# Optimization experiments

Hardware: AMD Instinct MI355X
Metric: run time of the kernel (lower is better)

The kernel has to match this reference:

```python
import jax, jax.numpy as jnp
import numpy as np

N = 4096          # n_assets
D_MODEL = 512
DK = 128
EMB_DIM = 32
QC = 4.0          # quantization_coeff
NUM_EMB = int(np.floor((N - 1) / QC)) + 1  # 1024


def setup_inputs() -> dict:
    key = jax.random.key(0)
    ks = jax.random.split(key, 9)

    def lin_w(k, out_d, in_d):
        # torch nn.Linear default init ~ U(-1/sqrt(in_d), 1/sqrt(in_d))
        b = 1.0 / np.sqrt(in_d)
        return jax.random.uniform(k, (out_d, in_d), jnp.float32, -b, b)

    return {
        "stock_reprs": jax.random.normal(ks[0], (N, D_MODEL), jnp.float32),
        "price_rising_ranks": jax.random.uniform(ks[1], (N,), jnp.float32, 0.0, float(N)),
        "Wq_w": lin_w(ks[2], DK, D_MODEL), "Wq_b": jnp.zeros((DK,), jnp.float32),
        "Wk_w": lin_w(ks[3], DK, D_MODEL), "Wk_b": jnp.zeros((DK,), jnp.float32),
        "Wv_w": lin_w(ks[4], D_MODEL, D_MODEL), "Wv_b": jnp.zeros((D_MODEL,), jnp.float32),
        "rank_emb": jax.random.normal(ks[5], (NUM_EMB, EMB_DIM), jnp.float32),
        "wL_w": lin_w(ks[6], 1, EMB_DIM), "wL_b": jnp.zeros((1,), jnp.float32),
        "wf_w": lin_w(ks[7], 1, D_MODEL), "wf_b": jnp.zeros((1,), jnp.float32),
    }


def reference(stock_reprs, price_rising_ranks, Wq_w, Wq_b, Wk_w, Wk_b,
              Wv_w, Wv_b, rank_emb, wL_w, wL_b, wf_w, wf_b):
    # QKV projections: [N, dk], [N, dk], [N, d_model]
    q = stock_reprs @ Wq_w.T + Wq_b
    k = stock_reprs @ Wk_w.T + Wk_b
    v = stock_reprs @ Wv_w.T + Wv_b

    # Quantized pairwise rank-distance indices [N, N]
    diff = jnp.abs(price_rising_ranks[:, None] - price_rising_ranks[None, :])
    d_ij = jnp.clip(jnp.floor(diff / QC).astype(jnp.int32), 0, NUM_EMB - 1)

    # Gate per quantized distance: sigmoid(w_L(Emb[d])). Precompute the
    # [NUM_EMB] table instead of materializing the [N, N, EMB_DIM] gather
    # (same math: the lookup-then-linear commutes with the gather).
    gate_table = jax.nn.sigmoid(rank_emb @ wL_w[0] + wL_b[0])  # [NUM_EMB]
    psi = gate_table[d_ij]                                     # [N, N]

    score = (q @ k.T) / np.sqrt(float(DK))                     # [N, N]
    att = jax.nn.softmax(psi * score, axis=-1)                 # [N, N]
    a = att @ v                                                # [N, d_model]
    return jax.nn.sigmoid(a @ wf_w[0] + wf_b[0])               # [N]
```

## Files before the change

### kernel.cpp

```cpp
#include <hip/hip_runtime.h>
#include <hip/hip_bf16.h>

#define N_ASSETS 4096
#define DMODEL 512
#define DKQ 128
#define NUM_EMB 1024

#define SCLQ 0.12752789f

typedef float f32x4 __attribute__((ext_vector_type(4)));
typedef short s16x8 __attribute__((ext_vector_type(8)));

__device__ __forceinline__ unsigned short f2bf(float x) {
    unsigned u = __float_as_uint(x);
    u += 0x7FFF + ((u >> 16) & 1);
    return (unsigned short)(u >> 16);
}

__device__ __forceinline__ unsigned pk2(float lo, float hi) {
    __hip_bfloat162 h = __float22bfloat162_rn(make_float2(lo, hi));
    return *(unsigned*)&h;
}

__device__ __forceinline__ s16x8 ld8(const unsigned short* p) {
    return *(const s16x8*)p;
}

__global__ __launch_bounds__(256) void k_prep(const float* __restrict__ remb,
                                              const float* __restrict__ wLw,
                                              const float* __restrict__ wLb,
                                              const float* __restrict__ Wq,
                                              const float* __restrict__ Wk,
                                              const float* __restrict__ bq,
                                              const float* __restrict__ bk,
                                              const float* __restrict__ Wv,
                                              const float* __restrict__ bv,
                                              const float* __restrict__ wfw,
                                              float* __restrict__ gate,
                                              unsigned short* __restrict__ Wb,
                                              float* __restrict__ bias,
                                              float* __restrict__ weff4) {
    int bid = blockIdx.x;
    int tid = threadIdx.x;
    if (bid < 4) {
        int e = bid * 256 + tid;
        float s = wLb[0];
#pragma unroll
        for (int j = 0; j < 32; ++j) s += remb[e * 32 + j] * wLw[j];
        gate[e] = 1.f / (1.f + __expf(-s));
    } else if (bid < 132) {
        int gid = (bid - 4) * 256 + tid;
        int i4 = gid * 4;
        int row = i4 >> 9;
        int col = i4 & 511;
        const float* src; int r;
        if (row < 128) { src = Wq; r = row; } else { src = Wk; r = row - 128; }
        float4 v = *(const float4*)(src + r * 512 + col);
        ushort4 o;
        o.x = f2bf(v.x); o.y = f2bf(v.y); o.z = f2bf(v.z); o.w = f2bf(v.w);
        *(ushort4*)(Wb + i4) = o;
        if (gid < 256) bias[gid] = (gid < 128) ? bq[gid] : bk[gid - 128];
    } else if (bid < 136) {
        int dbase = (bid - 132) * 128;
        float a0 = 0.f, a1 = 0.f;
        const float* wp = Wv + (size_t)dbase * 512 + tid * 2;
#pragma unroll 8
        for (int j = 0; j < 128; ++j) {
            float wfv = wfw[dbase + j];
            float2 v = *(const float2*)(wp + (size_t)j * 512);
            a0 += v.x * wfv;
            a1 += v.y * wfv;
        }
        weff4[(bid - 132) * 512 + tid * 2] = a0;
        weff4[(bid - 132) * 512 + tid * 2 + 1] = a1;
    } else {
        if (tid < 64) {
            float s = 0.f;
#pragma unroll
            for (int j = 0; j < 8; ++j) s += bv[tid * 8 + j] * wfw[tid * 8 + j];
#pragma unroll
            for (int m = 1; m < 64; m <<= 1) s += __shfl_xor(s, m);
            if (tid == 0) weff4[2048] = s;
        }
    }
}

__global__ __launch_bounds__(256) void k_proj(const float* __restrict__ X,
                                              const float* __restrict__ weff4,
                                              const unsigned short* __restrict__ Wb,
                                              const float* __restrict__ bias,
                                              unsigned short* __restrict__ qb,
                                              unsigned short* __restrict__ kb,
                                              float* __restrict__ u) {
    int tid = threadIdx.x;
    int lane = tid & 63, w = tid >> 6;
    int l15 = lane & 15, lhi = lane >> 4;
    int m0 = blockIdx.x * 16;
    int n0w = blockIdx.y * 128 + w * 32;

    const float* xrow = X + (size_t)(m0 + l15) * DMODEL + lhi * 8;

    s16x8 af[16];
    float us = 0.f;
    bool dou = (w == 0) && (blockIdx.y == 0);
#pragma unroll
    for (int kc = 0; kc < 16; ++kc) {
        float4 a = *(const float4*)(xrow + kc * 32);
        float4 b = *(const float4*)(xrow + kc * 32 + 4);
        if (dou) {
            int off = kc * 32 + lhi * 8;
            float4 p0 = *(const float4*)(weff4 + off);
            float4 p1 = *(const float4*)(weff4 + 512 + off);
            float4 p2 = *(const float4*)(weff4 + 1024 + off);
            float4 p3 = *(const float4*)(weff4 + 1536 + off);
            float4 q0 = *(const float4*)(weff4 + off + 4);
            float4 q1 = *(const float4*)(weff4 + 512 + off + 4);
            float4 q2 = *(const float4*)(weff4 + 1024 + off + 4);
            float4 q3 = *(const float4*)(weff4 + 1536 + off + 4);
            float wax = p0.x + p1.x + p2.x + p3.x;
            float way = p0.y + p1.y + p2.y + p3.y;
            float waz = p0.z + p1.z + p2.z + p3.z;
            float waw = p0.w + p1.w + p2.w + p3.w;
            float wbx = q0.x + q1.x + q2.x + q3.x;
            float wby = q0.y + q1.y + q2.y + q3.y;
            float wbz = q0.z + q1.z + q2.z + q3.z;
            float wbw = q0.w + q1.w + q2.w + q3.w;
            us += a.x * wax + a.y * way + a.z * waz + a.w * waw
                + b.x * wbx + b.y * wby + b.z * wbz + b.w * wbw;
        }
        union { s16x8 v; unsigned q[4]; } fr;
        fr.q[0] = pk2(a.x, a.y);
        fr.q[1] = pk2(a.z, a.w);
        fr.q[2] = pk2(b.x, b.y);
        fr.q[3] = pk2(b.z, b.w);
        af[kc] = fr.v;
    }
    if (dou) {
        us += __shfl_xor(us, 16);
        us += __shfl_xor(us, 32);
        if (lane < 16) u[m0 + lane] = us + weff4[2048];
    }

    f32x4 zero4 = {0.f, 0.f, 0.f, 0.f};
    f32x4 acc[2];
#pragma unroll
    for (int ni = 0; ni < 2; ++ni) acc[ni] = zero4;

#pragma unroll
    for (int k0 = 0; k0 < 16; ++k0) {
#pragma unroll
        for (int ni = 0; ni < 2; ++ni) {
            s16x8 bf = ld8(Wb + (size_t)(n0w + ni * 16 + l15) * 512 + k0 * 32 + lhi * 8);
            acc[ni] = __builtin_amdgcn_mfma_f32_16x16x32_bf16(af[k0], bf, acc[ni], 0, 0, 0);
        }
    }

#pragma unroll
    for (int ni = 0; ni < 2; ++ni) {
        int n = n0w + ni * 16 + l15;
        float bv_ = bias[n];
#pragma unroll
        for (int r = 0; r < 4; ++r) {
            int m = m0 + lhi * 4 + r;
            float v = acc[ni][r] + bv_;
            if (n < 128) qb[m * 128 + n] = f2bf(v * SCLQ);
            else         kb[m * 128 + (n - 128)] = f2bf(v);
        }
    }
}

__global__ __launch_bounds__(256) void k_score(const unsigned short* __restrict__ qb,
                                               const unsigned short* __restrict__ kb,
                                               const float* __restrict__ ranks,
                                               const float* __restrict__ gate,
                                               const float* __restrict__ u,
                                               float* __restrict__ num_part,
                                               float* __restrict__ den_part) {
    __shared__ float g_lds[NUM_EMB];
    __shared__ float rr[128], rc[128], uc[128];
    int tid = threadIdx.x;
    int lane = tid & 63, w = tid >> 6;
    int l15 = lane & 15, lhi = lane >> 4;
    int wm = w >> 1, wn = w & 1;
    int bm = blockIdx.x, bn = blockIdx.y;

    for (int i = tid; i < NUM_EMB; i += 256) g_lds[i] = gate[i];
    if (tid < 128) {
        rr[tid] = ranks[bm * 128 + tid];
        rc[tid] = ranks[bn * 128 + tid];
        uc[tid] = u[bn * 128 + tid];
    }
    __syncthreads();

    int row0 = wm * 64;
    int col0 = wn * 64;

    f32x4 zero4 = {0.f, 0.f, 0.f, 0.f};
    f32x4 acc[4][4];
#pragma unroll
    for (int mi = 0; mi < 4; ++mi)
#pragma unroll
        for (int ni = 0; ni < 4; ++ni) acc[mi][ni] = zero4;

#pragma unroll
    for (int k0 = 0; k0 < DKQ; k0 += 32) {
        s16x8 af[4], bf[4];
#pragma unroll
        for (int mi = 0; mi < 4; ++mi)
            af[mi] = ld8(qb + (bm * 128 + row0 + mi * 16 + l15) * DKQ + k0 + lhi * 8);
#pragma unroll
        for (int ni = 0; ni < 4; ++ni)
            bf[ni] = ld8(kb + (bn * 128 + col0 + ni * 16 + l15) * DKQ + k0 + lhi * 8);
#pragma unroll
        for (int mi = 0; mi < 4; ++mi)
#pragma unroll
            for (int ni = 0; ni < 4; ++ni)
                acc[mi][ni] = __builtin_amdgcn_mfma_f32_16x16x32_bf16(af[mi], bf[ni], acc[mi][ni], 0, 0, 0);
    }

    float rreg[4][4];
#pragma unroll
    for (int mi = 0; mi < 4; ++mi)
#pragma unroll
        for (int r = 0; r < 4; ++r) rreg[mi][r] = rr[row0 + mi * 16 + lhi * 4 + r];

    float num[4][4], den[4][4];
#pragma unroll
    for (int mi = 0; mi < 4; ++mi)
#pragma unroll
        for (int r = 0; r < 4; ++r) { num[mi][r] = 0.f; den[mi][r] = 0.f; }

#pragma unroll
    for (int mi = 0; mi < 4; ++mi) {
#pragma unroll
        for (int ni = 0; ni < 4; ++ni) {
            int coll = col0 + ni * 16 + l15;
            float rj = rc[coll];
            float uj = uc[coll];
#pragma unroll
            for (int r = 0; r < 4; ++r) {
                float diff = fabsf(rreg[mi][r] - rj);
                int d = min((int)(diff * 0.25f), NUM_EMB - 1);
                float p = exp2f(g_lds[d] * acc[mi][ni][r]);
                den[mi][r] += p;
                num[mi][r] += p * uj;
            }
        }
    }
    int slot = bn * 2 + wn;
#pragma unroll
    for (int mi = 0; mi < 4; ++mi) {
#pragma unroll
        for (int r = 0; r < 4; ++r) {
            float vn = num[mi][r], vd = den[mi][r];
            vn += __shfl_xor(vn, 1); vd += __shfl_xor(vd, 1);
            vn += __shfl_xor(vn, 2); vd += __shfl_xor(vd, 2);
            vn += __shfl_xor(vn, 4); vd += __shfl_xor(vd, 4);
            vn += __shfl_xor(vn, 8); vd += __shfl_xor(vd, 8);
            if (l15 == 0) {
                int row = bm * 128 + row0 + mi * 16 + lhi * 4 + r;
                num_part[row * 64 + slot] = vn;
                den_part[row * 64 + slot] = vd;
            }
        }
    }
}

__global__ __launch_bounds__(256) void k_out(const float* __restrict__ num_part,
                                             const float* __restrict__ den_part,
                                             const float* __restrict__ wfb,
                                             float* __restrict__ out) {
    int lane = threadIdx.x & 63, w = threadIdx.x >> 6;
    int row = blockIdx.x * 4 + w;
    float vn = num_part[row * 64 + lane];
    float vd = den_part[row * 64 + lane];
#pragma unroll
    for (int m = 1; m < 64; m <<= 1) {
        vn += __shfl_xor(vn, m);
        vd += __shfl_xor(vd, m);
    }
    if (lane == 0) out[row] = 1.f / (1.f + __expf(-(vn / vd + wfb[0])));
}

extern "C" void kernel_launch(void* const* d_in, const int* in_sizes, int n_in,
                              void* d_out, int out_size, void* d_ws, size_t ws_size,
                              hipStream_t stream) {
    const float* X    = (const float*)d_in[0];
    const float* rks  = (const float*)d_in[1];
    const float* Wq_w = (const float*)d_in[2];
    const float* Wq_b = (const float*)d_in[3];
    const float* Wk_w = (const float*)d_in[4];
    const float* Wk_b = (const float*)d_in[5];
    const float* Wv_w = (const float*)d_in[6];
    const float* Wv_b = (const float*)d_in[7];
    const float* remb = (const float*)d_in[8];
    const float* wL_w = (const float*)d_in[9];
    const float* wL_b = (const float*)d_in[10];
    const float* wf_w = (const float*)d_in[11];
    const float* wf_b = (const float*)d_in[12];
    float* out = (float*)d_out;
    char* ws = (char*)d_ws;

    const size_t OFF_GATE  = 0;
    const size_t OFF_BIAS  = 4096;
    const size_t OFF_WEFF4 = 8192;
    const size_t OFF_WB    = 20480;
    const size_t OFF_QB    = OFF_WB + 262144;
    const size_t OFF_KB    = OFF_QB + 1048576;
    const size_t OFF_U     = OFF_KB + 1048576;
    const size_t OFF_NUM   = OFF_U + 16384;
    const size_t OFF_DEN   = OFF_NUM + 1048576;

    float* gate = (float*)(ws + OFF_GATE);
    float* bias = (float*)(ws + OFF_BIAS);
    float* weff4 = (float*)(ws + OFF_WEFF4);
    unsigned short* Wb = (unsigned short*)(ws + OFF_WB);
    unsigned short* qb = (unsigned short*)(ws + OFF_QB);
    unsigned short* kb = (unsigned short*)(ws + OFF_KB);
    float* u = (float*)(ws + OFF_U);
    float* num_part = (float*)(ws + OFF_NUM);
    float* den_part = (float*)(ws + OFF_DEN);

    k_prep<<<137, 256, 0, stream>>>(remb, wL_w, wL_b, Wq_w, Wk_w, Wq_b, Wk_b,
                                    Wv_w, Wv_b, wf_w, gate, Wb, bias, weff4);
    k_proj<<<dim3(256, 2), 256, 0, stream>>>(X, weff4, Wb, bias, qb, kb, u);
    k_score<<<dim3(32, 32), 256, 0, stream>>>(qb, kb, rks, gate, u, num_part, den_part);
    k_out<<<1024, 256, 0, stream>>>(num_part, den_part, wf_b, out);
}
```

Before: 60.18 us.

## Fuse final row reduction into score kernel via last-block atomic counter

Removes the separate k_out launch. Each score block bumps a per-row-block atomic counter, and the last of the 32 column blocks reduces the partial num/den sums and writes the sigmoid output, which needs a memset of the counters first. Also pre-scales the ranks by 0.25 so the quantised index is just the truncated absolute difference, dropping the min clamp, and splits the Wv·wf prep across more blocks so it runs in more parallel.

```diff
diff --git a/kernel.cpp b/kernel.cpp
--- a/kernel.cpp
+++ b/kernel.cpp
@@ -60,19 +60,20 @@
         o.x = f2bf(v.x); o.y = f2bf(v.y); o.z = f2bf(v.z); o.w = f2bf(v.w);
         *(ushort4*)(Wb + i4) = o;
         if (gid < 256) bias[gid] = (gid < 128) ? bq[gid] : bk[gid - 128];
-    } else if (bid < 136) {
-        int dbase = (bid - 132) * 128;
-        float a0 = 0.f, a1 = 0.f;
-        const float* wp = Wv + (size_t)dbase * 512 + tid * 2;
+    } else if (bid < 148) {
+        int r = bid - 132;
+        int s = r >> 2;
+        int q = r & 3;
+        if (tid < 128) {
+            int din = q * 128 + tid;
+            int dbase = s * 128;
+            const float* wp = Wv + (size_t)dbase * 512 + din;
+            float a = 0.f;
 #pragma unroll 8
-        for (int j = 0; j < 128; ++j) {
-            float wfv = wfw[dbase + j];
-            float2 v = *(const float2*)(wp + (size_t)j * 512);
-            a0 += v.x * wfv;
-            a1 += v.y * wfv;
-        }
-        weff4[(bid - 132) * 512 + tid * 2] = a0;
-        weff4[(bid - 132) * 512 + tid * 2 + 1] = a1;
+            for (int j = 0; j < 128; ++j)
+                a += wp[(size_t)j * 512] * wfw[dbase + j];
+            weff4[s * 512 + din] = a;
+        }
     } else {
         if (tid < 64) {
             float s = 0.f;
@@ -175,9 +176,13 @@
                                                const float* __restrict__ gate,
                                                const float* __restrict__ u,
                                                float* __restrict__ num_part,
-                                               float* __restrict__ den_part) {
+                                               float* __restrict__ den_part,
+                                               int* __restrict__ cnt,
+                                               const float* __restrict__ wfb,
+                                               float* __restrict__ out) {
     __shared__ float g_lds[NUM_EMB];
     __shared__ float rr[128], rc[128], uc[128];
+    __shared__ int lastflag;
     int tid = threadIdx.x;
     int lane = tid & 63, w = tid >> 6;
     int l15 = lane & 15, lhi = lane >> 4;
@@ -186,8 +191,8 @@
 
     for (int i = tid; i < NUM_EMB; i += 256) g_lds[i] = gate[i];
     if (tid < 128) {
-        rr[tid] = ranks[bm * 128 + tid];
-        rc[tid] = ranks[bn * 128 + tid];
+        rr[tid] = ranks[bm * 128 + tid] * 0.25f;
+        rc[tid] = ranks[bn * 128 + tid] * 0.25f;
         uc[tid] = u[bn * 128 + tid];
     }
     __syncthreads();
@@ -239,8 +244,7 @@
             float uj = uc[coll];
 #pragma unroll
             for (int r = 0; r < 4; ++r) {
-                float diff = fabsf(rreg[mi][r] - rj);
-                int d = min((int)(diff * 0.25f), NUM_EMB - 1);
+                int d = (int)fabsf(rreg[mi][r] - rj);
                 float p = exp2f(g_lds[d] * acc[mi][ni][r]);
                 den[mi][r] += p;
                 num[mi][r] += p * uj;
@@ -264,22 +268,31 @@
             }
         }
     }
-}
-
-__global__ __launch_bounds__(256) void k_out(const float* __restrict__ num_part,
-                                             const float* __restrict__ den_part,
-                                             const float* __restrict__ wfb,
-                                             float* __restrict__ out) {
-    int lane = threadIdx.x & 63, w = threadIdx.x >> 6;
-    int row = blockIdx.x * 4 + w;
-    float vn = num_part[row * 64 + lane];
-    float vd = den_part[row * 64 + lane];
-#pragma unroll
-    for (int m = 1; m < 64; m <<= 1) {
-        vn += __shfl_xor(vn, m);
-        vd += __shfl_xor(vd, m);
-    }
-    if (lane == 0) out[row] = 1.f / (1.f + __expf(-(vn / vd + wfb[0])));
+
+    __threadfence();
+    __syncthreads();
+    if (tid == 0) {
+        int old = __hip_atomic_fetch_add(&cnt[bm], 1, __ATOMIC_ACQ_REL,
+                                         __HIP_MEMORY_SCOPE_AGENT);
+        lastflag = (old == 31);
+    }
+    __syncthreads();
+    if (lastflag) {
+        __threadfence();
+        float wfb0 = wfb[0];
+        int rl0 = w * 32;
+        for (int rl = rl0; rl < rl0 + 32; ++rl) {
+            int row = bm * 128 + rl;
+            float vn = num_part[row * 64 + lane];
+            float vd = den_part[row * 64 + lane];
+#pragma unroll
+            for (int m = 1; m < 64; m <<= 1) {
+                vn += __shfl_xor(vn, m);
+                vd += __shfl_xor(vd, m);
+            }
+            if (lane == 0) out[row] = 1.f / (1.f + __expf(-(vn / vd + wfb0)));
+        }
+    }
 }
 
 extern "C" void kernel_launch(void* const* d_in, const int* in_sizes, int n_in,
@@ -310,6 +323,7 @@
     const size_t OFF_U     = OFF_KB + 1048576;
     const size_t OFF_NUM   = OFF_U + 16384;
     const size_t OFF_DEN   = OFF_NUM + 1048576;
+    const size_t OFF_CNT   = OFF_DEN + 1048576;
 
     float* gate = (float*)(ws + OFF_GATE);
     float* bias = (float*)(ws + OFF_BIAS);
@@ -320,10 +334,12 @@
     float* u = (float*)(ws + OFF_U);
     float* num_part = (float*)(ws + OFF_NUM);
     float* den_part = (float*)(ws + OFF_DEN);
-
-    k_prep<<<137, 256, 0, stream>>>(remb, wL_w, wL_b, Wq_w, Wk_w, Wq_b, Wk_b,
+    int* cnt = (int*)(ws + OFF_CNT);
+
+    hipMemsetAsync(cnt, 0, 32 * sizeof(int), stream);
+    k_prep<<<149, 256, 0, stream>>>(remb, wL_w, wL_b, Wq_w, Wk_w, Wq_b, Wk_b,
                                     Wv_w, Wv_b, wf_w, gate, Wb, bias, weff4);
     k_proj<<<dim3(256, 2), 256, 0, stream>>>(X, weff4, Wb, bias, qb, kb, u);
-    k_score<<<dim3(32, 32), 256, 0, stream>>>(qb, kb, rks, gate, u, num_part, den_part);
-    k_out<<<1024, 256, 0, stream>>>(num_part, den_part, wf_b, out);
-}
+    k_score<<<dim3(32, 32), 256, 0, stream>>>(qb, kb, rks, gate, u, num_part,
+                                              den_part, cnt, wf_b, out);
+}
```

Result: slower. 203.1 us (+237.5%).
